# Kernel tuning notes

Hardware: AMD Instinct MI355X
Metric: run time of the kernel (lower is better)

Reference implementation:

```python
import jax, jax.numpy as jnp
import numpy as np

N = 50000      # total batched graph nodes (both ASTs of all examples)
E = 30000      # edges per edge type
T = 8          # num edge types (no master node, no sibling edges)
H = 128        # gnn hidden = change_vector_dim // 2
TAG = 32       # change-tag embed size
CONTENT = H - TAG
VOCAB = 20000  # rows of token/content encoding table
B = 64         # num examples
STEPS = (3, 3) # layer_time_steps


def setup_inputs() -> dict:
    key = jax.random.key(0)
    ks = jax.random.split(key, 22)
    s = 0.05
    inp = {}
    inp["node_content_ids"] = jax.random.randint(ks[0], (N,), 0, VOCAB)
    inp["node_tag_ids"] = jax.random.randint(ks[1], (N,), 0, 4)
    inp["edge_src"] = jax.random.randint(ks[2], (T, E), 0, N)
    inp["edge_tgt"] = jax.random.randint(ks[3], (T, E), 0, N)
    inp["node2example"] = jnp.sort(jax.random.randint(ks[4], (N,), 0, B))
    inp["content_table"] = jax.random.normal(ks[5], (VOCAB, CONTENT)) * s
    inp["tag_embedding"] = jax.random.normal(ks[6], (4, TAG)) * s
    inp["msg_W"] = jax.random.normal(ks[7], (2, T, H, H)) * s
    inp["msg_b"] = jax.random.normal(ks[8], (2, T, H)) * s
    inp["gru0_Wih"] = jax.random.normal(ks[9], (H, 3 * H)) * s
    inp["gru0_Whh"] = jax.random.normal(ks[10], (H, 3 * H)) * s
    inp["gru0_bih"] = jax.random.normal(ks[11], (3 * H,)) * s
    inp["gru0_bhh"] = jax.random.normal(ks[12], (3 * H,)) * s
    inp["gru1_Wih"] = jax.random.normal(ks[13], (2 * H, 3 * H)) * s  # layer 1 gets residual concat -> 2H input
    inp["gru1_Whh"] = jax.random.normal(ks[14], (H, 3 * H)) * s
    inp["gru1_bih"] = jax.random.normal(ks[15], (3 * H,)) * s
    inp["gru1_bhh"] = jax.random.normal(ks[16], (3 * H,)) * s
    inp["r1_w"] = jax.random.normal(ks[17], (H,)) * s
    inp["r1_b"] = jax.random.normal(ks[18], ()) * s
    inp["r2_w"] = jax.random.normal(ks[19], (H,)) * s
    inp["r2_b"] = jax.random.normal(ks[20], ()) * s
    return inp


def _gru(x, h, Wih, Whh, bih, bhh):
    # PyTorch GRUCell gate order: r, z, n
    gi = x @ Wih + bih
    gh = h @ Whh + bhh
    i_r, i_z, i_n = jnp.split(gi, 3, axis=-1)
    h_r, h_z, h_n = jnp.split(gh, 3, axis=-1)
    r = jax.nn.sigmoid(i_r + h_r)
    z = jax.nn.sigmoid(i_z + h_z)
    n = jnp.tanh(i_n + r * h_n)
    return (1.0 - z) * n + z * h


def reference(node_content_ids, node_tag_ids, edge_src, edge_tgt, node2example,
              content_table, tag_embedding, msg_W, msg_b,
              gru0_Wih, gru0_Whh, gru0_bih, gru0_bhh,
              gru1_Wih, gru1_Whh, gru1_bih, gru1_bhh,
              r1_w, r1_b, r2_w, r2_b):
    # init node embeddings: [token/content encoding || change-tag embedding] -> [N, H]
    init = jnp.concatenate([content_table[node_content_ids],
                            tag_embedding[node_tag_ids]], axis=-1)
    states = init
    layer_out = []
    for layer, steps in enumerate(STEPS):
        for _ in range(steps):
            src_states = states[edge_src]                                   # [T,E,H] gather
            msgs = jnp.einsum('teh,thd->ted', src_states, msg_W[layer]) \
                   + msg_b[layer][:, None, :]                               # per-edge-type linear
            agg = jnp.zeros_like(states).at[edge_tgt].add(msgs)             # scatter-add to targets
            if layer == 1:
                # residual_connections={1:[0]}: concat initial states with incoming messages
                x = jnp.concatenate([init, agg], axis=-1)
                states = _gru(x, states, gru1_Wih, gru1_Whh, gru1_bih, gru1_bhh)
            else:
                states = _gru(agg, states, gru0_Wih, gru0_Whh, gru0_bih, gru0_bhh)
        layer_out.append(states)
    s1, s2 = layer_out
    # gated scalar readout per layer, pooled per example, concatenated -> [B, 2H]
    g1 = jax.nn.sigmoid(s1 @ r1_w + r1_b)[:, None]
    g2 = jax.nn.sigmoid(s2 @ r2_w + r2_b)[:, None]
    pooled1 = jax.ops.segment_sum(g1 * s1, node2example, num_segments=B)
    pooled2 = jax.ops.segment_sum(g2 * s2, node2example, num_segments=B)
    return jnp.concatenate([pooled1, pooled2], axis=-1)
```

## Files before the change

### kernel.cpp

```cpp
#include <hip/hip_runtime.h>
#include <hip/hip_bf16.h>

#define NN 50000
#define NE 30000
#define NT 8
#define HH 128
#define NB 64
#define CONT 96
#define TPB 16
#define EDGES (NT * NE)
#define SBLK 512
#define SNB ((NN + SBLK - 1) / SBLK)
#define RCH 8
#define NTILE (NN / 16)
#define NPAIR ((NTILE + 1) / 2)
#define XB ((NPAIR + 3) / 4)
#define GPERS 768

typedef __attribute__((ext_vector_type(8))) short short8;
typedef __attribute__((ext_vector_type(4))) float f32x4;

__device__ __forceinline__ float sigm(float x) { return 1.f / (1.f + __expf(-x)); }
__device__ __forceinline__ float tanhf_fast(float x) {
  float e = __expf(2.f * x);
  return 1.f - 2.f / (e + 1.f);
}
__device__ __forceinline__ unsigned short bfbits(float x) {
  __hip_bfloat16 b = __float2bfloat16(x);
  return *(unsigned short*)&b;
}

__global__ __launch_bounds__(256) void init_kernel(
    const int* __restrict__ cid, const int* __restrict__ tg,
    const float* __restrict__ ctab, const float* __restrict__ ttab,
    __hip_bfloat16* __restrict__ sbf, __hip_bfloat16* __restrict__ ibf)
{
  int i = blockIdx.x * 256 + threadIdx.x;
  if (i >= NN * HH) return;
  int n = i >> 7, d = i & 127;
  float v;
  if (d < CONT) v = ctab[(size_t)cid[n] * CONT + d];
  else          v = ttab[(size_t)tg[n] * 32 + (d - CONT)];
  __hip_bfloat16 b = __float2bfloat16(v);
  sbf[i] = b;
  ibf[i] = b;
}

__global__ __launch_bounds__(256) void hist_kernel(
    const int* __restrict__ etgt, int* __restrict__ cnt)
{
  int i = blockIdx.x * 256 + threadIdx.x;
  if (i >= EDGES) return;
  atomicAdd(&cnt[etgt[i]], 1);
}

__global__ __launch_bounds__(SBLK) void scanA_kernel(
    const int* __restrict__ cnt, int* __restrict__ row_ptr, int* __restrict__ bsum)
{
  __shared__ int sm[SBLK];
  const int tid = threadIdx.x;
  const int i = blockIdx.x * SBLK + tid;
  int v = (i < NN) ? cnt[i] : 0;
  sm[tid] = v;
  __syncthreads();
  for (int off = 1; off < SBLK; off <<= 1) {
    int t = (tid >= off) ? sm[tid - off] : 0;
    __syncthreads();
    sm[tid] += t;
    __syncthreads();
  }
  if (i < NN) row_ptr[i] = sm[tid] - v;
  if (tid == SBLK - 1) bsum[blockIdx.x] = sm[tid];
}

__global__ __launch_bounds__(128) void scanB_kernel(
    const int* __restrict__ bsum, int* __restrict__ boff, int* __restrict__ row_ptr,
    const int* __restrict__ n2e, int* __restrict__ ebnd)
{
  __shared__ int sm[128];
  const int tid = threadIdx.x;
  int v = (tid < SNB) ? bsum[tid] : 0;
  sm[tid] = v;
  __syncthreads();
  for (int off = 1; off < 128; off <<= 1) {
    int t = (tid >= off) ? sm[tid - off] : 0;
    __syncthreads();
    sm[tid] += t;
    __syncthreads();
  }
  if (tid < SNB) boff[tid] = sm[tid] - v;
  if (tid == 127) row_ptr[NN] = sm[127];
  if (tid <= NB) {
    int lo = 0, hi = NN;
    while (lo < hi) { int mid = (lo + hi) >> 1; if (n2e[mid] < tid) lo = mid + 1; else hi = mid; }
    ebnd[tid] = lo;
  }
}

__global__ __launch_bounds__(SBLK) void scanC_kernel(
    int* __restrict__ row_ptr, int* __restrict__ cnt2, const int* __restrict__ boff)
{
  int i = blockIdx.x * SBLK + threadIdx.x;
  if (i >= NN) return;
  int r = row_ptr[i] + boff[blockIdx.x];
  row_ptr[i] = r;
  cnt2[i] = r;
}

__global__ __launch_bounds__(256) void scatter_kernel(
    const int* __restrict__ etgt, int* __restrict__ cnt2, int* __restrict__ perm)
{
  int i = blockIdx.x * 256 + threadIdx.x;
  if (i >= EDGES) return;
  perm[i] = atomicAdd(&cnt2[etgt[i]], 1);
}

__device__ __forceinline__ void gru_swz_one(
    const float* __restrict__ W, __hip_bfloat16* __restrict__ out, int KSL, int mode, int i)
{
  int j = i & 7, lane = (i >> 3) & 63, kk = (i >> 9) % KSL, nt = i / (KSL * 512);
  int hi = lane >> 4, lo = lane & 15;
  int p = kk * 32 + hi * 8 + j;
  int k;
  if (mode == 0)      k = p;
  else if (mode == 1) k = (p & 7) * 16 + (p >> 3);
  else                k = (p < 128) ? p : 128 + ((p - 128) & 7) * 16 + ((p - 128) >> 3);
  out[i] = __float2bfloat16(W[(size_t)k * 384 + nt * 16 + lo]);
}

__global__ __launch_bounds__(256) void wswz_all_kernel(
    const float* __restrict__ msgW, __hip_bfloat16* __restrict__ wswz,
    const float* __restrict__ g0Wih, __hip_bfloat16* __restrict__ w0ih,
    const float* __restrict__ g0Whh, __hip_bfloat16* __restrict__ w0hh,
    const float* __restrict__ g1Wih, __hip_bfloat16* __restrict__ w1ih,
    const float* __restrict__ g1Whh, __hip_bfloat16* __restrict__ w1hh)
{
  int i = blockIdx.x * 256 + threadIdx.x;
  if (i < 262144) {
    int j = i & 7, lane = (i >> 3) & 63, kk = (i >> 9) & 3, nt = (i >> 11) & 7, lt = i >> 14;
    int hi = lane >> 4, lo = lane & 15;
    int k = kk * 32 + hi * 8 + j;
    wswz[i] = __float2bfloat16(msgW[((size_t)lt * HH + k) * HH + nt * 16 + lo]);
    return;
  }
  i -= 262144;
  if (i < 49152)  { gru_swz_one(g0Wih, w0ih, 4, 1, i); return; }
  i -= 49152;
  if (i < 49152)  { gru_swz_one(g0Whh, w0hh, 4, 0, i); return; }
  i -= 49152;
  if (i < 98304)  { gru_swz_one(g1Wih, w1ih, 8, 2, i); return; }
  i -= 98304;
  if (i < 49152)  { gru_swz_one(g1Whh, w1hh, 4, 0, i); return; }
}

__global__ __launch_bounds__(256) void msg_mfma_kernel(
    const __hip_bfloat16* __restrict__ sbf, const int* __restrict__ esrc,
    const int* __restrict__ perm, const __hip_bfloat16* __restrict__ wswz,
    const float* __restrict__ ball, __hip_bfloat16* __restrict__ msgs, int layer)
{
  __shared__ short8 Wl[8 * 4 * 64];
  const int t = blockIdx.y;
  {
    const float4* wg = (const float4*)(wswz + (size_t)(layer * NT + t) * 16384);
    float4* wl = (float4*)Wl;
    for (int i = threadIdx.x; i < 2048; i += 256) wl[i] = wg[i];
  }
  const int lane = threadIdx.x & 63;
  const int wv   = threadIdx.x >> 6;
  const int hi = lane >> 4, lo = lane & 15;
  float bias_v[8];
#pragma unroll
  for (int nt = 0; nt < 8; ++nt)
    bias_v[nt] = ball[(layer * NT + t) * HH + nt * 16 + lo];
  __syncthreads();

  const int tile_end = min((int)(blockIdx.x + 1) * TPB, NE / 16);
  for (int tile = blockIdx.x * TPB + wv; tile < tile_end; tile += 4) {
    const int e0 = tile * 16;
    const int src = esrc[t * NE + e0 + lo];
    const short* srow = (const short*)(sbf + (size_t)src * HH);
    short8 a[4];
#pragma unroll
    for (int kk = 0; kk < 4; ++kk)
      a[kk] = *(const short8*)(srow + kk * 32 + hi * 8);
    int slot[4];
#pragma unroll
    for (int r = 0; r < 4; ++r) slot[r] = perm[t * NE + e0 + hi * 4 + r];
    f32x4 acc[8];
#pragma unroll
    for (int nt = 0; nt < 8; ++nt) acc[nt] = (f32x4){0.f, 0.f, 0.f, 0.f};
#pragma unroll
    for (int nt = 0; nt < 8; ++nt)
#pragma unroll
      for (int kk = 0; kk < 4; ++kk)
        acc[nt] = __builtin_amdgcn_mfma_f32_16x16x32_bf16(
            a[kk], Wl[(nt * 4 + kk) * 64 + lane], acc[nt], 0, 0, 0);
#pragma unroll
    for (int r = 0; r < 4; ++r) {
      short8 m;
#pragma unroll
      for (int nt = 0; nt < 8; ++nt)
        ((unsigned short*)&m)[nt] = bfbits(acc[nt][r] + bias_v[nt]);
      *(short8*)((short*)msgs + (size_t)slot[r] * HH + lo * 8) = m;
    }
  }
}

__global__ __launch_bounds__(256) void reduce_kernel(
    const __hip_bfloat16* __restrict__ msgs, const int* __restrict__ row_ptr,
    __hip_bfloat16* __restrict__ agg)
{
  const int lane = threadIdx.x & 63;
  const int n = blockIdx.x * 4 + (threadIdx.x >> 6);
  if (n >= NN) return;
  const int b = row_ptr[n], e = row_ptr[n + 1];
  float a0 = 0.f, a1 = 0.f;
  for (int i = b; i < e; ++i) {
    unsigned int v = *(const unsigned int*)((const short*)msgs + (size_t)i * HH + lane * 2);
    a0 += __uint_as_float(v << 16);
    a1 += __uint_as_float(v & 0xffff0000u);
  }
  unsigned int o = ((unsigned int)bfbits(a1) << 16) | bfbits(a0);
  *(unsigned int*)((short*)agg + (size_t)n * HH + lane * 2) = o;
}

template <int KSL, int DTG>
__global__ __launch_bounds__(256) void gru_mfma_kernel(
    const __hip_bfloat16* __restrict__ agg,
    const __hip_bfloat16* __restrict__ ibf,
    const __hip_bfloat16* __restrict__ hbf,
    const __hip_bfloat16* __restrict__ Wih_s,
    const __hip_bfloat16* __restrict__ Whh_s,
    const float* __restrict__ bih, const float* __restrict__ bhh,
    __hip_bfloat16* __restrict__ sbf_out)
{
  constexpr int D2 = 8 / DTG;
  constexpr int NSLOT = GPERS / (8 * DTG);
  const int b = blockIdx.x;
  const int xcd = b & 7;
  const int dtg = (b >> 3) & (DTG - 1);
  const int slot = b / (8 * DTG);

  __shared__ short8 BihL[D2 * 3 * KSL * 64];
  {
    const short8* Bih_g = (const short8*)Wih_s;
    for (int i = threadIdx.x; i < D2 * 3 * KSL * 64; i += 256) {
      int lane_i = i & 63, kk = (i >> 6) % KSL, g = ((i >> 6) / KSL) % 3, d2 = (i >> 6) / (KSL * 3);
      BihL[i] = Bih_g[((size_t)(dtg * D2 + d2 + 8 * g) * KSL + kk) * 64 + lane_i];
    }
  }
  const int lane = threadIdx.x & 63;
  const int wv   = threadIdx.x >> 6;
  const int hi = lane >> 4, lo = lane & 15;
  float birv[D2], bizv[D2], binv[D2], bhrv[D2], bhzv[D2], bhnv[D2];
#pragma unroll
  for (int d2 = 0; d2 < D2; ++d2) {
    const int c = (dtg * D2 + d2) * 16 + lo;
    birv[d2] = bih[c]; bizv[d2] = bih[c + 128]; binv[d2] = bih[c + 256];
    bhrv[d2] = bhh[c]; bhzv[d2] = bhh[c + 128]; bhnv[d2] = bhh[c + 256];
  }
  __syncthreads();

  const short8* __restrict__ Bhh_g = (const short8*)Whh_s;

  for (int xb = xcd + 8 * slot; xb < XB; xb += 8 * NSLOT) {
    const int pt = xb * 4 + wv;
    if (pt >= NPAIR) continue;
    const int t0 = pt * 2;
    const bool two = (t0 + 1 < NTILE);

    short8 ax[2][KSL], ah[2][4];
#pragma unroll
    for (int u = 0; u < 2; ++u) {
      const int nb = ((u && two) ? t0 + 1 : t0) * 16;
      const short* arow = (const short*)(agg + (size_t)(nb + lo) * HH);
      const short* hrow = (const short*)(hbf + (size_t)(nb + lo) * HH);
      if (KSL == 8) {
        const short* irow = (const short*)(ibf + (size_t)(nb + lo) * HH);
#pragma unroll
        for (int kk = 0; kk < 4; ++kk) {
          ax[u][kk]     = *(const short8*)(irow + kk * 32 + hi * 8);
          ax[u][kk + 4] = *(const short8*)(arow + kk * 32 + hi * 8);
        }
      } else {
#pragma unroll
        for (int kk = 0; kk < KSL; ++kk)
          ax[u][kk] = *(const short8*)(arow + kk * 32 + hi * 8);
      }
#pragma unroll
      for (int kk = 0; kk < 4; ++kk)
        ah[u][kk] = *(const short8*)(hrow + kk * 32 + hi * 8);
    }

#pragma unroll
    for (int d2 = 0; d2 < D2; ++d2) {
      const int dt = dtg * D2 + d2;
      f32x4 aR[2], aZ[2], aNi[2], aNh[2];
#pragma unroll
      for (int u = 0; u < 2; ++u) {
        aR[u] = (f32x4){0.f, 0.f, 0.f, 0.f};
        aZ[u] = (f32x4){0.f, 0.f, 0.f, 0.f};
        aNi[u] = (f32x4){0.f, 0.f, 0.f, 0.f};
        aNh[u] = (f32x4){0.f, 0.f, 0.f, 0.f};
      }
#pragma unroll
      for (int kk = 0; kk < KSL; ++kk) {
        short8 br = BihL[((d2 * 3 + 0) * KSL + kk) * 64 + lane];
        short8 bz = BihL[((d2 * 3 + 1) * KSL + kk) * 64 + lane];
        short8 bn = BihL[((d2 * 3 + 2) * KSL + kk) * 64 + lane];
#pragma unroll
        for (int u = 0; u < 2; ++u) {
          aR[u]  = __builtin_amdgcn_mfma_f32_16x16x32_bf16(ax[u][kk], br, aR[u], 0, 0, 0);
          aZ[u]  = __builtin_amdgcn_mfma_f32_16x16x32_bf16(ax[u][kk], bz, aZ[u], 0, 0, 0);
          aNi[u] = __builtin_amdgcn_mfma_f32_16x16x32_bf16(ax[u][kk], bn, aNi[u], 0, 0, 0);
        }
      }
#pragma unroll
      for (int kk = 0; kk < 4; ++kk) {
        short8 br = Bhh_g[((size_t)(dt     ) * 4 + kk) * 64 + lane];
        short8 bz = Bhh_g[((size_t)(dt +  8) * 4 + kk) * 64 + lane];
        short8 bn = Bhh_g[((size_t)(dt + 16) * 4 + kk) * 64 + lane];
#pragma unroll
        for (int u = 0; u < 2; ++u) {
          aR[u]  = __builtin_amdgcn_mfma_f32_16x16x32_bf16(ah[u][kk], br, aR[u], 0, 0, 0);
          aZ[u]  = __builtin_amdgcn_mfma_f32_16x16x32_bf16(ah[u][kk], bz, aZ[u], 0, 0, 0);
          aNh[u] = __builtin_amdgcn_mfma_f32_16x16x32_bf16(ah[u][kk], bn, aNh[u], 0, 0, 0);
        }
      }
      const int c = dt * 16 + lo;
      const int uend = two ? 2 : 1;
      for (int u = 0; u < uend; ++u) {
        const int nb = (t0 + u) * 16;
#pragma unroll
        for (int r = 0; r < 4; ++r) {
          const int node = nb + hi * 4 + r;
          const float rg = sigm(aR[u][r] + birv[d2] + bhrv[d2]);
          const float zg = sigm(aZ[u][r] + bizv[d2] + bhzv[d2]);
          const float ng = tanhf_fast(aNi[u][r] + binv[d2] + rg * (aNh[u][r] + bhnv[d2]));
          const float hc = __bfloat162float(hbf[(size_t)node * HH + c]);
          sbf_out[(size_t)node * HH + c] = __float2bfloat16((1.f - zg) * ng + zg * hc);
        }
      }
    }
  }
}

__global__ __launch_bounds__(256) void readout_kernel(
    const __hip_bfloat16* __restrict__ sbf, const int* __restrict__ ebnd,
    const float* __restrict__ rw, const float* __restrict__ rb,
    float* __restrict__ out, int coff)
{
  __shared__ float sm[4][128];
  const int ex = blockIdx.x / RCH, ch = blockIdx.x % RCH;
  const int s = ebnd[ex], e = ebnd[ex + 1];
  const int lane = threadIdx.x & 63;
  const int wv   = threadIdx.x >> 6;
  const float w0 = rw[2 * lane], w1 = rw[2 * lane + 1], rbv = rb[0];
  float a0 = 0.f, a1 = 0.f;
  for (int n = s + ch * 4 + wv; n < e; n += 4 * RCH) {
    unsigned int v = *(const unsigned int*)((const short*)sbf + (size_t)n * HH + lane * 2);
    const float s0 = __uint_as_float(v << 16);
    const float s1 = __uint_as_float(v & 0xffff0000u);
    float p = s0 * w0 + s1 * w1;
#pragma unroll
    for (int o = 32; o; o >>= 1) p += __shfl_xor(p, o, 64);
    const float g = sigm(p + rbv);
    a0 += g * s0;
    a1 += g * s1;
  }
  sm[wv][2 * lane] = a0;
  sm[wv][2 * lane + 1] = a1;
  __syncthreads();
  if (wv == 0) {
    const int c0 = 2 * lane, c1 = 2 * lane + 1;
    float v0 = sm[0][c0] + sm[1][c0] + sm[2][c0] + sm[3][c0];
    float v1 = sm[0][c1] + sm[1][c1] + sm[2][c1] + sm[3][c1];
    atomicAdd(&out[(size_t)ex * (2 * HH) + coff + c0], v0);
    atomicAdd(&out[(size_t)ex * (2 * HH) + coff + c1], v1);
  }
}

extern "C" void kernel_launch(void* const* d_in, const int* in_sizes, int n_in,
                              void* d_out, int out_size, void* d_ws, size_t ws_size,
                              hipStream_t stream)
{
  const int*   cid   = (const int*)d_in[0];
  const int*   tg    = (const int*)d_in[1];
  const int*   esrc  = (const int*)d_in[2];
  const int*   etgt  = (const int*)d_in[3];
  const int*   n2e   = (const int*)d_in[4];
  const float* ctab  = (const float*)d_in[5];
  const float* ttab  = (const float*)d_in[6];
  const float* msgW  = (const float*)d_in[7];
  const float* msgb  = (const float*)d_in[8];
  const float* g0Wih = (const float*)d_in[9];
  const float* g0Whh = (const float*)d_in[10];
  const float* g0bih = (const float*)d_in[11];
  const float* g0bhh = (const float*)d_in[12];
  const float* g1Wih = (const float*)d_in[13];
  const float* g1Whh = (const float*)d_in[14];
  const float* g1bih = (const float*)d_in[15];
  const float* g1bhh = (const float*)d_in[16];
  const float* r1w   = (const float*)d_in[17];
  const float* r1b   = (const float*)d_in[18];
  const float* r2w   = (const float*)d_in[19];
  const float* r2b   = (const float*)d_in[20];

  float* out = (float*)d_out;
  __hip_bfloat16* sb0  = (__hip_bfloat16*)d_ws;
  __hip_bfloat16* sb1  = sb0 + (size_t)NN * HH;
  __hip_bfloat16* ibf  = sb1 + (size_t)NN * HH;
  __hip_bfloat16* agg  = ibf + (size_t)NN * HH;
  __hip_bfloat16* msgs = agg + (size_t)NN * HH;
  __hip_bfloat16* wswz = msgs + (size_t)EDGES * HH;
  __hip_bfloat16* w0ih = wswz + 262144;
  __hip_bfloat16* w0hh = w0ih + 24 * 4 * 512;
  __hip_bfloat16* w1ih = w0hh + 24 * 4 * 512;
  __hip_bfloat16* w1hh = w1ih + 24 * 8 * 512;
  int* row_ptr = (int*)(w1hh + 24 * 4 * 512);
  int* cnt     = row_ptr + NN + 1;
  int* cnt2    = cnt + NN;
  int* perm    = cnt2 + NN;
  int* bsum    = perm + EDGES;
  int* boff    = bsum + SNB;
  int* ebnd    = boff + SNB;

  hipMemsetAsync(d_out, 0, (size_t)NB * 2 * HH * sizeof(float), stream);
  hipMemsetAsync(cnt, 0, (size_t)NN * sizeof(int), stream);
  const int eblocks = (EDGES + 255) / 256;
  hist_kernel<<<eblocks, 256, 0, stream>>>(etgt, cnt);
  scanA_kernel<<<SNB, SBLK, 0, stream>>>(cnt, row_ptr, bsum);
  scanB_kernel<<<1, 128, 0, stream>>>(bsum, boff, row_ptr, n2e, ebnd);
  scanC_kernel<<<SNB, SBLK, 0, stream>>>(row_ptr, cnt2, boff);
  scatter_kernel<<<eblocks, 256, 0, stream>>>(etgt, cnt2, perm);

  wswz_all_kernel<<<507904 / 256, 256, 0, stream>>>(msgW, wswz, g0Wih, w0ih, g0Whh, w0hh,
                                                    g1Wih, w1ih, g1Whh, w1hh);
  init_kernel<<<(NN * HH + 255) / 256, 256, 0, stream>>>(cid, tg, ctab, ttab, sb0, ibf);

  dim3 mgrid((NE / 16 + TPB - 1) / TPB, NT);
  const int rblocks = (NN + 3) / 4;
  __hip_bfloat16* cur = sb0;
  __hip_bfloat16* nxt = sb1;
  for (int s = 0; s < 3; ++s) {
    msg_mfma_kernel<<<mgrid, 256, 0, stream>>>(cur, esrc, perm, wswz, msgb, msgs, 0);
    reduce_kernel<<<rblocks, 256, 0, stream>>>(msgs, row_ptr, agg);
    gru_mfma_kernel<4, 2><<<GPERS, 256, 0, stream>>>(agg, ibf, cur, w0ih, w0hh,
                                                     g0bih, g0bhh, nxt);
    __hip_bfloat16* t = cur; cur = nxt; nxt = t;
  }
  readout_kernel<<<NB * RCH, 256, 0, stream>>>(cur, ebnd, r1w, r1b, out, 0);

  for (int s = 0; s < 3; ++s) {
    msg_mfma_kernel<<<mgrid, 256, 0, stream>>>(cur, esrc, perm, wswz, msgb, msgs, 1);
    reduce_kernel<<<rblocks, 256, 0, stream>>>(msgs, row_ptr, agg);
    gru_mfma_kernel<8, 4><<<GPERS, 256, 0, stream>>>(agg, ibf, cur, w1ih, w1hh,
                                                     g1bih, g1bhh, nxt);
    __hip_bfloat16* t = cur; cur = nxt; nxt = t;
  }
  readout_kernel<<<NB * RCH, 256, 0, stream>>>(cur, ebnd, r2w, r2b, out, HH);
}
```

Before: 647.1 us.

## Replace persistent GRU grid with one-shot 512-thread blocks over fixed output-column groups

The GRU kernel drops the persistent grid-stride loop over node pairs. It now launches a non-persistent grid of 512-thread blocks where each block handles 8 wave-pairs of tiles for one group of two 16-column output tiles. Every block loads a smaller shared Wih slice covering only 2 column tiles. The intent is to cut per-wave serial work and improve latency hiding through more concurrent waves, at the cost of reloading the weight slice into shared memory in every block.

```diff
diff --git a/kernel.cpp b/kernel.cpp
--- a/kernel.cpp
+++ b/kernel.cpp
@@ -14,8 +14,8 @@
 #define RCH 8
 #define NTILE (NN / 16)
 #define NPAIR ((NTILE + 1) / 2)
-#define XB ((NPAIR + 3) / 4)
-#define GPERS 768
+#define XB8 ((NPAIR + 7) / 8)
+#define GGRID8 (((XB8 + 7) / 8) * 32)
 
 typedef __attribute__((ext_vector_type(8))) short short8;
 typedef __attribute__((ext_vector_type(4))) float f32x4;
@@ -224,8 +224,8 @@
   *(unsigned int*)((short*)agg + (size_t)n * HH + lane * 2) = o;
 }
 
-template <int KSL, int DTG>
-__global__ __launch_bounds__(256) void gru_mfma_kernel(
+template <int KSL>
+__global__ __launch_bounds__(512) void gru_mfma_kernel(
     const __hip_bfloat16* __restrict__ agg,
     const __hip_bfloat16* __restrict__ ibf,
     const __hip_bfloat16* __restrict__ hbf,
@@ -234,112 +234,108 @@
     const float* __restrict__ bih, const float* __restrict__ bhh,
     __hip_bfloat16* __restrict__ sbf_out)
 {
-  constexpr int D2 = 8 / DTG;
-  constexpr int NSLOT = GPERS / (8 * DTG);
-  const int b = blockIdx.x;
-  const int xcd = b & 7;
-  const int dtg = (b >> 3) & (DTG - 1);
-  const int slot = b / (8 * DTG);
-
-  __shared__ short8 BihL[D2 * 3 * KSL * 64];
+  const int wg = blockIdx.x;
+  const int xb = (wg >> 5) * 8 + (wg & 7);
+  const int dtg = (wg >> 3) & 3;
+  if (xb >= XB8) return;
+
+  __shared__ short8 BihL[2 * 3 * KSL * 64];
   {
     const short8* Bih_g = (const short8*)Wih_s;
-    for (int i = threadIdx.x; i < D2 * 3 * KSL * 64; i += 256) {
+    for (int i = threadIdx.x; i < 2 * 3 * KSL * 64; i += 512) {
       int lane_i = i & 63, kk = (i >> 6) % KSL, g = ((i >> 6) / KSL) % 3, d2 = (i >> 6) / (KSL * 3);
-      BihL[i] = Bih_g[((size_t)(dtg * D2 + d2 + 8 * g) * KSL + kk) * 64 + lane_i];
+      BihL[i] = Bih_g[((size_t)(dtg * 2 + d2 + 8 * g) * KSL + kk) * 64 + lane_i];
     }
   }
   const int lane = threadIdx.x & 63;
   const int wv   = threadIdx.x >> 6;
   const int hi = lane >> 4, lo = lane & 15;
-  float birv[D2], bizv[D2], binv[D2], bhrv[D2], bhzv[D2], bhnv[D2];
-#pragma unroll
-  for (int d2 = 0; d2 < D2; ++d2) {
-    const int c = (dtg * D2 + d2) * 16 + lo;
+  float birv[2], bizv[2], binv[2], bhrv[2], bhzv[2], bhnv[2];
+#pragma unroll
+  for (int d2 = 0; d2 < 2; ++d2) {
+    const int c = (dtg * 2 + d2) * 16 + lo;
     birv[d2] = bih[c]; bizv[d2] = bih[c + 128]; binv[d2] = bih[c + 256];
     bhrv[d2] = bhh[c]; bhzv[d2] = bhh[c + 128]; bhnv[d2] = bhh[c + 256];
   }
   __syncthreads();
 
+  const int pt = xb * 8 + wv;
+  if (pt >= NPAIR) return;
+  const int t0 = pt * 2;
+  const bool two = (t0 + 1 < NTILE);
+
+  short8 ax[2][KSL], ah[2][4];
+#pragma unroll
+  for (int u = 0; u < 2; ++u) {
+    const int nb = ((u && two) ? t0 + 1 : t0) * 16;
+    const short* arow = (const short*)(agg + (size_t)(nb + lo) * HH);
+    const short* hrow = (const short*)(hbf + (size_t)(nb + lo) * HH);
+    if (KSL == 8) {
+      const short* irow = (const short*)(ibf + (size_t)(nb + lo) * HH);
+#pragma unroll
+      for (int kk = 0; kk < 4; ++kk) {
+        ax[u][kk]     = *(const short8*)(irow + kk * 32 + hi * 8);
+        ax[u][kk + 4] = *(const short8*)(arow + kk * 32 + hi * 8);
+      }
+    } else {
+#pragma unroll
+      for (int kk = 0; kk < KSL; ++kk)
+        ax[u][kk] = *(const short8*)(arow + kk * 32 + hi * 8);
+    }
+#pragma unroll
+    for (int kk = 0; kk < 4; ++kk)
+      ah[u][kk] = *(const short8*)(hrow + kk * 32 + hi * 8);
+  }
+
   const short8* __restrict__ Bhh_g = (const short8*)Whh_s;
 
-  for (int xb = xcd + 8 * slot; xb < XB; xb += 8 * NSLOT) {
-    const int pt = xb * 4 + wv;
-    if (pt >= NPAIR) continue;
-    const int t0 = pt * 2;
-    const bool two = (t0 + 1 < NTILE);
-
-    short8 ax[2][KSL], ah[2][4];
+#pragma unroll
+  for (int d2 = 0; d2 < 2; ++d2) {
+    const int dt = dtg * 2 + d2;
+    f32x4 aR[2], aZ[2], aNi[2], aNh[2];
 #pragma unroll
     for (int u = 0; u < 2; ++u) {
-      const int nb = ((u && two) ? t0 + 1 : t0) * 16;
-      const short* arow = (const short*)(agg + (size_t)(nb + lo) * HH);
-      const short* hrow = (const short*)(hbf + (size_t)(nb + lo) * HH);
-      if (KSL == 8) {
-        const short* irow = (const short*)(ibf + (size_t)(nb + lo) * HH);
-#pragma unroll
-        for (int kk = 0; kk < 4; ++kk) {
-          ax[u][kk]     = *(const short8*)(irow + kk * 32 + hi * 8);
-          ax[u][kk + 4] = *(const short8*)(arow + kk * 32 + hi * 8);
-        }
-      } else {
-#pragma unroll
-        for (int kk = 0; kk < KSL; ++kk)
-          ax[u][kk] = *(const short8*)(arow + kk * 32 + hi * 8);
+      aR[u] = (f32x4){0.f, 0.f, 0.f, 0.f};
+      aZ[u] = (f32x4){0.f, 0.f, 0.f, 0.f};
+      aNi[u] = (f32x4){0.f, 0.f, 0.f, 0.f};
+      aNh[u] = (f32x4){0.f, 0.f, 0.f, 0.f};
+    }
+#pragma unroll
+    for (int kk = 0; kk < KSL; ++kk) {
+      short8 br = BihL[((d2 * 3 + 0) * KSL + kk) * 64 + lane];
+      short8 bz = BihL[((d2 * 3 + 1) * KSL + kk) * 64 + lane];
+      short8 bn = BihL[((d2 * 3 + 2) * KSL + kk) * 64 + lane];
+#pragma unroll
+      for (int u = 0; u < 2; ++u) {
+        aR[u]  = __builtin_amdgcn_mfma_f32_16x16x32_bf16(ax[u][kk], br, aR[u], 0, 0, 0);
+        aZ[u]  = __builtin_amdgcn_mfma_f32_16x16x32_bf16(ax[u][kk], bz, aZ[u], 0, 0, 0);
+        aNi[u] = __builtin_amdgcn_mfma_f32_16x16x32_bf16(ax[u][kk], bn, aNi[u], 0, 0, 0);
       }
-#pragma unroll
-      for (int kk = 0; kk < 4; ++kk)
-        ah[u][kk] = *(const short8*)(hrow + kk * 32 + hi * 8);
-    }
-
-#pragma unroll
-    for (int d2 = 0; d2 < D2; ++d2) {
-      const int dt = dtg * D2 + d2;
-      f32x4 aR[2], aZ[2], aNi[2], aNh[2];
+    }
+#pragma unroll
+    for (int kk = 0; kk < 4; ++kk) {
+      short8 br = Bhh_g[((size_t)(dt     ) * 4 + kk) * 64 + lane];
+      short8 bz = Bhh_g[((size_t)(dt +  8) * 4 + kk) * 64 + lane];
+      short8 bn = Bhh_g[((size_t)(dt + 16) * 4 + kk) * 64 + lane];
 #pragma unroll
       for (int u = 0; u < 2; ++u) {
-        aR[u] = (f32x4){0.f, 0.f, 0.f, 0.f};
-        aZ[u] = (f32x4){0.f, 0.f, 0.f, 0.f};
-        aNi[u] = (f32x4){0.f, 0.f, 0.f, 0.f};
-        aNh[u] = (f32x4){0.f, 0.f, 0.f, 0.f};
+        aR[u]  = __builtin_amdgcn_mfma_f32_16x16x32_bf16(ah[u][kk], br, aR[u], 0, 0, 0);
+        aZ[u]  = __builtin_amdgcn_mfma_f32_16x16x32_bf16(ah[u][kk], bz, aZ[u], 0, 0, 0);
+        aNh[u] = __builtin_amdgcn_mfma_f32_16x16x32_bf16(ah[u][kk], bn, aNh[u], 0, 0, 0);
       }
-#pragma unroll
-      for (int kk = 0; kk < KSL; ++kk) {
-        short8 br = BihL[((d2 * 3 + 0) * KSL + kk) * 64 + lane];
-        short8 bz = BihL[((d2 * 3 + 1) * KSL + kk) * 64 + lane];
-        short8 bn = BihL[((d2 * 3 + 2) * KSL + kk) * 64 + lane];
-#pragma unroll
-        for (int u = 0; u < 2; ++u) {
-          aR[u]  = __builtin_amdgcn_mfma_f32_16x16x32_bf16(ax[u][kk], br, aR[u], 0, 0, 0);
-          aZ[u]  = __builtin_amdgcn_mfma_f32_16x16x32_bf16(ax[u][kk], bz, aZ[u], 0, 0, 0);
-          aNi[u] = __builtin_amdgcn_mfma_f32_16x16x32_bf16(ax[u][kk], bn, aNi[u], 0, 0, 0);
-        }
-      }
-#pragma unroll
-      for (int kk = 0; kk < 4; ++kk) {
-        short8 br = Bhh_g[((size_t)(dt     ) * 4 + kk) * 64 + lane];
-        short8 bz = Bhh_g[((size_t)(dt +  8) * 4 + kk) * 64 + lane];
-        short8 bn = Bhh_g[((size_t)(dt + 16) * 4 + kk) * 64 + lane];
-#pragma unroll
-        for (int u = 0; u < 2; ++u) {
-          aR[u]  = __builtin_amdgcn_mfma_f32_16x16x32_bf16(ah[u][kk], br, aR[u], 0, 0, 0);
-          aZ[u]  = __builtin_amdgcn_mfma_f32_16x16x32_bf16(ah[u][kk], bz, aZ[u], 0, 0, 0);
-          aNh[u] = __builtin_amdgcn_mfma_f32_16x16x32_bf16(ah[u][kk], bn, aNh[u], 0, 0, 0);
-        }
-      }
-      const int c = dt * 16 + lo;
-      const int uend = two ? 2 : 1;
-      for (int u = 0; u < uend; ++u) {
-        const int nb = (t0 + u) * 16;
-#pragma unroll
-        for (int r = 0; r < 4; ++r) {
-          const int node = nb + hi * 4 + r;
-          const float rg = sigm(aR[u][r] + birv[d2] + bhrv[d2]);
-          const float zg = sigm(aZ[u][r] + bizv[d2] + bhzv[d2]);
-          const float ng = tanhf_fast(aNi[u][r] + binv[d2] + rg * (aNh[u][r] + bhnv[d2]));
-          const float hc = __bfloat162float(hbf[(size_t)node * HH + c]);
-          sbf_out[(size_t)node * HH + c] = __float2bfloat16((1.f - zg) * ng + zg * hc);
-        }
+    }
+    const int c = dt * 16 + lo;
+    const int uend = two ? 2 : 1;
+    for (int u = 0; u < uend; ++u) {
+      const int nb = (t0 + u) * 16;
+#pragma unroll
+      for (int r = 0; r < 4; ++r) {
+        const int node = nb + hi * 4 + r;
+        const float rg = sigm(aR[u][r] + birv[d2] + bhrv[d2]);
+        const float zg = sigm(aZ[u][r] + bizv[d2] + bhzv[d2]);
+        const float ng = tanhf_fast(aNi[u][r] + binv[d2] + rg * (aNh[u][r] + bhnv[d2]));
+        const float hc = __bfloat162float(hbf[(size_t)node * HH + c]);
+        sbf_out[(size_t)node * HH + c] = __float2bfloat16((1.f - zg) * ng + zg * hc);
       }
     }
   }
@@ -445,8 +441,8 @@
   for (int s = 0; s < 3; ++s) {
     msg_mfma_kernel<<<mgrid, 256, 0, stream>>>(cur, esrc, perm, wswz, msgb, msgs, 0);
     reduce_kernel<<<rblocks, 256, 0, stream>>>(msgs, row_ptr, agg);
-    gru_mfma_kernel<4, 2><<<GPERS, 256, 0, stream>>>(agg, ibf, cur, w0ih, w0hh,
-                                                     g0bih, g0bhh, nxt);
+    gru_mfma_kernel<4><<<GGRID8, 512, 0, stream>>>(agg, ibf, cur, w0ih, w0hh,
+                                                   g0bih, g0bhh, nxt);
     __hip_bfloat16* t = cur; cur = nxt; nxt = t;
   }
   readout_kernel<<<NB * RCH, 256, 0, stream>>>(cur, ebnd, r1w, r1b, out, 0);
@@ -454,8 +450,8 @@
   for (int s = 0; s < 3; ++s) {
     msg_mfma_kernel<<<mgrid, 256, 0, stream>>>(cur, esrc, perm, wswz, msgb, msgs, 1);
     reduce_kernel<<<rblocks, 256, 0, stream>>>(msgs, row_ptr, agg);
-    gru_mfma_kernel<8, 4><<<GPERS, 256, 0, stream>>>(agg, ibf, cur, w1ih, w1hh,
-                                                     g1bih, g1bhh, nxt);
+    gru_mfma_kernel<8><<<GGRID8, 512, 0, stream>>>(agg, ibf, cur, w1ih, w1hh,
+                                                   g1bih, g1bhh, nxt);
     __hip_bfloat16* t = cur; cur = nxt; nxt = t;
   }
   readout_kernel<<<NB * RCH, 256, 0, stream>>>(cur, ebnd, r2w, r2b, out, HH);
```

Measured after the change: 657.5 us. No clear change (+1.6%).
